# Kernel optimization log

Hardware: AMD Instinct MI355X
Metric: run time of the kernel (lower is better)

The kernel has to match this reference:

```python
import jax, jax.numpy as jnp
import numpy as np
import math

U_CONST = 0.5
FAC_DECAY = math.exp(-1.0 / 100.0)  # tau_fac = 100
DEP_DECAY = math.exp(-1.0 / 200.0)  # tau_dep = 200
BATCH, IN_F, OUT_F = 8192, 4096, 128


def setup_inputs() -> dict:
    key = jax.random.key(0)
    k1, k2 = jax.random.split(key)
    # binary spikes in {0,1} as float32
    pre_spike = jax.random.randint(k1, (BATCH, IN_F), 0, 2).astype(jnp.float32)
    # weight ~ U[0.25, 0.75) per torch.rand(out,in)*0.5 + 0.25
    weight = jax.random.uniform(k2, (OUT_F, IN_F), dtype=jnp.float32) * 0.5 + 0.25
    u = jnp.full((BATCH, IN_F), U_CONST, dtype=jnp.float32)  # facilitation state
    x = jnp.ones((BATCH, IN_F), dtype=jnp.float32)           # depression state
    return {"pre_spike": pre_spike, "weight": weight, "u": u, "x": x}


def reference(pre_spike, weight, u, x):
    # release probability per (batch, in_feature); fold onto pre_spike instead of
    # materializing the (batch, out, in) effective weight (same math).
    release_prob = u * x
    out = jnp.einsum('bi,oi->bo', pre_spike * release_prob, weight)  # [B, out]

    # STP state updates (facilitation then depression; x-update uses NEW u)
    u_fd = u * FAC_DECAY
    u_new = u_fd + U_CONST * (1.0 - u_fd) * pre_spike
    x_new = x * DEP_DECAY + (1.0 - x) * DEP_DECAY * (1.0 - pre_spike * u_new)
    return out, u_new, x_new
```

## Files before the change

kernel.cpp:

```cpp
#include <hip/hip_runtime.h>
#include <hip/hip_bf16.h>
#include <cstdint>

#define BATCH 8192
#define IN_F  4096
#define OUT_F 128
#define KSPLIT 16
#define KSLICE (IN_F / KSPLIT)
#define NKS    (KSLICE / 32)
#define FD 0.99004983374916811f
#define DD 0.99501247919268232f

typedef __attribute__((ext_vector_type(4))) float f32x4;
typedef __attribute__((ext_vector_type(8))) float f32x8;
typedef __attribute__((ext_vector_type(8))) short bf16x8;

__device__ __forceinline__ unsigned short f2bf(float f){
  union { float f; unsigned u; } v; v.f = f;
  unsigned u = v.u;
  return (unsigned short)((u + 0x7FFFu + ((u >> 16) & 1u)) >> 16);
}

__global__ __launch_bounds__(256) void prep_weight_kernel(const float* __restrict__ w,
                                                          unsigned short* __restrict__ wf){
  const int f  = blockIdx.x * 256 + threadIdx.x;
  const int l  = f & 63;
  const int ct = (f >> 6) & 7;
  const int ks = f >> 9;
  const int row = ct * 16 + (l & 15);
  const int k   = ks * 32 + ((l >> 4) << 3);
  const f32x4* src = reinterpret_cast<const f32x4*>(w + (size_t)row * IN_F + k);
  f32x4 a = src[0], b = src[1];
  union { bf16x8 v; unsigned short s[8]; } o;
  o.s[0]=f2bf(a[0]); o.s[1]=f2bf(a[1]); o.s[2]=f2bf(a[2]); o.s[3]=f2bf(a[3]);
  o.s[4]=f2bf(b[0]); o.s[5]=f2bf(b[1]); o.s[6]=f2bf(b[2]); o.s[7]=f2bf(b[3]);
  *reinterpret_cast<bf16x8*>(wf + (size_t)f * 8) = o.v;
}

template<bool WS>
__global__ __launch_bounds__(256, 4) void stp_fused_kernel(
    const float* __restrict__ pre, const float* __restrict__ uin,
    const float* __restrict__ xin, const float* __restrict__ w,
    const unsigned short* __restrict__ wf,
    float* __restrict__ out, float* __restrict__ un_out, float* __restrict__ xn_out)
{
  const int tid = threadIdx.x;
  const int wv  = tid >> 6;
  const int l   = tid & 63;

  const int kslice  = blockIdx.x & (KSPLIT - 1);
  const int rowBase = (blockIdx.x >> 4) * 64 + wv * 16;
  const int row     = rowBase + (l & 15);
  const size_t base = (size_t)row * IN_F + kslice * KSLICE + ((l >> 4) << 3);

  f32x4 acc[8];
  #pragma unroll
  for (int ct = 0; ct < 8; ++ct) acc[ct] = (f32x4){0.f,0.f,0.f,0.f};

  f32x8 sC = *reinterpret_cast<const f32x8*>(pre + base);
  f32x8 uC = *reinterpret_cast<const f32x8*>(uin + base);
  f32x8 xC = *reinterpret_cast<const f32x8*>(xin + base);

  for (int ks = 0; ks < NKS; ++ks){
    const size_t g   = base + (size_t)(ks << 5);
    const int    gks = kslice * NKS + ks;

    bf16x8 bf[8];
    if (WS){
      const bf16x8* wfp = reinterpret_cast<const bf16x8*>(wf);
      #pragma unroll
      for (int ct = 0; ct < 8; ++ct)
        bf[ct] = wfp[(size_t)((gks * 8 + ct) << 6) + l];
    } else {
      const int kg = gks * 32 + ((l >> 4) << 3);
      #pragma unroll
      for (int ct = 0; ct < 8; ++ct){
        const int r0 = ct * 16 + (l & 15);
        const f32x4* p = reinterpret_cast<const f32x4*>(w + (size_t)r0 * IN_F + kg);
        f32x4 a = p[0], b = p[1];
        union { bf16x8 v; unsigned short s[8]; } t;
        t.s[0]=f2bf(a[0]); t.s[1]=f2bf(a[1]); t.s[2]=f2bf(a[2]); t.s[3]=f2bf(a[3]);
        t.s[4]=f2bf(b[0]); t.s[5]=f2bf(b[1]); t.s[6]=f2bf(b[2]); t.s[7]=f2bf(b[3]);
        bf[ct] = t.v;
      }
    }

    f32x8 sN, uN, xN;
    if (ks + 1 < NKS){
      const size_t gn = base + (size_t)((ks + 1) << 5);
      sN = *reinterpret_cast<const f32x8*>(pre + gn);
      uN = *reinterpret_cast<const f32x8*>(uin + gn);
      xN = *reinterpret_cast<const f32x8*>(xin + gn);
    }

    f32x8 un, xn;
    union { bf16x8 v; unsigned short s[8]; } af;
    #pragma unroll
    for (int j = 0; j < 8; ++j){
      const float s = sC[j], u = uC[j], x = xC[j];
      af.s[j] = f2bf(u * x * s);
      const float ufd = u * FD;
      const float unj = ufd + 0.5f * (1.0f - ufd) * s;
      un[j] = unj;
      xn[j] = x * DD + (1.0f - x) * DD * (1.0f - s * unj);
    }
    *reinterpret_cast<f32x8*>(un_out + g) = un;
    *reinterpret_cast<f32x8*>(xn_out + g) = xn;

    #pragma unroll
    for (int ct = 0; ct < 8; ++ct)
      acc[ct] = __builtin_amdgcn_mfma_f32_16x16x32_bf16(af.v, bf[ct], acc[ct], 0, 0, 0);

    sC = sN; uC = uN; xC = xN;
  }

  const int col0 = l & 15;
  const int r0   = rowBase + ((l >> 4) << 2);
  #pragma unroll
  for (int ct = 0; ct < 8; ++ct){
    #pragma unroll
    for (int rg = 0; rg < 4; ++rg){
      unsafeAtomicAdd(&out[(size_t)(r0 + rg) * OUT_F + ct * 16 + col0], acc[ct][rg]);
    }
  }
}

extern "C" void kernel_launch(void* const* d_in, const int* in_sizes, int n_in,
                              void* d_out, int out_size, void* d_ws, size_t ws_size,
                              hipStream_t stream){
  const float* pre = (const float*)d_in[0];
  const float* w   = (const float*)d_in[1];
  const float* u   = (const float*)d_in[2];
  const float* x   = (const float*)d_in[3];
  float* out    = (float*)d_out;
  float* un_out = out + (size_t)BATCH * OUT_F;
  float* xn_out = un_out + (size_t)BATCH * IN_F;
  unsigned short* wf = (unsigned short*)d_ws;

  hipMemsetAsync(out, 0, (size_t)BATCH * OUT_F * sizeof(float), stream);

  const bool use_ws = (ws_size >= (size_t)(1 << 20));
  const int grid = (BATCH / 64) * KSPLIT;
  if (use_ws){
    prep_weight_kernel<<<256, 256, 0, stream>>>(w, wf);
    stp_fused_kernel<true><<<grid, 256, 0, stream>>>(pre, u, x, w, wf, out, un_out, xn_out);
  } else {
    stp_fused_kernel<false><<<grid, 256, 0, stream>>>(pre, u, x, w, nullptr, out, un_out, xn_out);
  }
}
```

Baseline: 187.7 us.

## Split K across waves in-block with LDS reduction, drop atomics and weight prep

After: 324.1 us. 1.73x slower.

```diff
diff --git a/kernel.cpp b/kernel.cpp
--- a/kernel.cpp
+++ b/kernel.cpp
@@ -5,9 +5,6 @@
 #define BATCH 8192
 #define IN_F  4096
 #define OUT_F 128
-#define KSPLIT 16
-#define KSLICE (IN_F / KSPLIT)
-#define NKS    (KSLICE / 32)
 #define FD 0.99004983374916811f
 #define DD 0.99501247919268232f
 
@@ -21,37 +18,18 @@
   return (unsigned short)((u + 0x7FFFu + ((u >> 16) & 1u)) >> 16);
 }
 
-__global__ __launch_bounds__(256) void prep_weight_kernel(const float* __restrict__ w,
-                                                          unsigned short* __restrict__ wf){
-  const int f  = blockIdx.x * 256 + threadIdx.x;
-  const int l  = f & 63;
-  const int ct = (f >> 6) & 7;
-  const int ks = f >> 9;
-  const int row = ct * 16 + (l & 15);
-  const int k   = ks * 32 + ((l >> 4) << 3);
-  const f32x4* src = reinterpret_cast<const f32x4*>(w + (size_t)row * IN_F + k);
-  f32x4 a = src[0], b = src[1];
-  union { bf16x8 v; unsigned short s[8]; } o;
-  o.s[0]=f2bf(a[0]); o.s[1]=f2bf(a[1]); o.s[2]=f2bf(a[2]); o.s[3]=f2bf(a[3]);
-  o.s[4]=f2bf(b[0]); o.s[5]=f2bf(b[1]); o.s[6]=f2bf(b[2]); o.s[7]=f2bf(b[3]);
-  *reinterpret_cast<bf16x8*>(wf + (size_t)f * 8) = o.v;
-}
-
-template<bool WS>
-__global__ __launch_bounds__(256, 4) void stp_fused_kernel(
+__global__ __launch_bounds__(512, 4) void stp_fused3(
     const float* __restrict__ pre, const float* __restrict__ uin,
     const float* __restrict__ xin, const float* __restrict__ w,
-    const unsigned short* __restrict__ wf,
     float* __restrict__ out, float* __restrict__ un_out, float* __restrict__ xn_out)
 {
+  __shared__ float red[8][16 * OUT_F];
+
   const int tid = threadIdx.x;
   const int wv  = tid >> 6;
   const int l   = tid & 63;
-
-  const int kslice  = blockIdx.x & (KSPLIT - 1);
-  const int rowBase = (blockIdx.x >> 4) * 64 + wv * 16;
-  const int row     = rowBase + (l & 15);
-  const size_t base = (size_t)row * IN_F + kslice * KSLICE + ((l >> 4) << 3);
+  const int rowBase = blockIdx.x * 16;
+  const size_t base = (size_t)(rowBase + (l & 15)) * IN_F + wv * 512 + ((l >> 4) << 3);
 
   f32x4 acc[8];
   #pragma unroll
@@ -61,33 +39,26 @@
   f32x8 uC = *reinterpret_cast<const f32x8*>(uin + base);
   f32x8 xC = *reinterpret_cast<const f32x8*>(xin + base);
 
-  for (int ks = 0; ks < NKS; ++ks){
+  for (int ks = 0; ks < 16; ++ks){
     const size_t g   = base + (size_t)(ks << 5);
-    const int    gks = kslice * NKS + ks;
+    const int    gks = (wv << 4) + ks;
+    const int    kg  = (gks << 5) + ((l >> 4) << 3);
 
     bf16x8 bf[8];
-    if (WS){
-      const bf16x8* wfp = reinterpret_cast<const bf16x8*>(wf);
-      #pragma unroll
-      for (int ct = 0; ct < 8; ++ct)
-        bf[ct] = wfp[(size_t)((gks * 8 + ct) << 6) + l];
-    } else {
-      const int kg = gks * 32 + ((l >> 4) << 3);
-      #pragma unroll
-      for (int ct = 0; ct < 8; ++ct){
-        const int r0 = ct * 16 + (l & 15);
-        const f32x4* p = reinterpret_cast<const f32x4*>(w + (size_t)r0 * IN_F + kg);
-        f32x4 a = p[0], b = p[1];
-        union { bf16x8 v; unsigned short s[8]; } t;
-        t.s[0]=f2bf(a[0]); t.s[1]=f2bf(a[1]); t.s[2]=f2bf(a[2]); t.s[3]=f2bf(a[3]);
-        t.s[4]=f2bf(b[0]); t.s[5]=f2bf(b[1]); t.s[6]=f2bf(b[2]); t.s[7]=f2bf(b[3]);
-        bf[ct] = t.v;
-      }
+    #pragma unroll
+    for (int ct = 0; ct < 8; ++ct){
+      const int r0 = ct * 16 + (l & 15);
+      const f32x4* p = reinterpret_cast<const f32x4*>(w + (size_t)r0 * IN_F + kg);
+      f32x4 a = p[0], b = p[1];
+      union { bf16x8 v; unsigned short s[8]; } t;
+      t.s[0]=f2bf(a[0]); t.s[1]=f2bf(a[1]); t.s[2]=f2bf(a[2]); t.s[3]=f2bf(a[3]);
+      t.s[4]=f2bf(b[0]); t.s[5]=f2bf(b[1]); t.s[6]=f2bf(b[2]); t.s[7]=f2bf(b[3]);
+      bf[ct] = t.v;
     }
 
     f32x8 sN, uN, xN;
-    if (ks + 1 < NKS){
-      const size_t gn = base + (size_t)((ks + 1) << 5);
+    if (ks < 15){
+      const size_t gn = g + 32;
       sN = *reinterpret_cast<const f32x8*>(pre + gn);
       uN = *reinterpret_cast<const f32x8*>(uin + gn);
       xN = *reinterpret_cast<const f32x8*>(xin + gn);
@@ -104,8 +75,8 @@
       un[j] = unj;
       xn[j] = x * DD + (1.0f - x) * DD * (1.0f - s * unj);
     }
-    *reinterpret_cast<f32x8*>(un_out + g) = un;
-    *reinterpret_cast<f32x8*>(xn_out + g) = xn;
+    __builtin_nontemporal_store(un, reinterpret_cast<f32x8*>(un_out + g));
+    __builtin_nontemporal_store(xn, reinterpret_cast<f32x8*>(xn_out + g));
 
     #pragma unroll
     for (int ct = 0; ct < 8; ++ct)
@@ -114,15 +85,21 @@
     sC = sN; uC = uN; xC = xN;
   }
 
-  const int col0 = l & 15;
-  const int r0   = rowBase + ((l >> 4) << 2);
   #pragma unroll
   for (int ct = 0; ct < 8; ++ct){
     #pragma unroll
     for (int rg = 0; rg < 4; ++rg){
-      unsafeAtomicAdd(&out[(size_t)(r0 + rg) * OUT_F + ct * 16 + col0], acc[ct][rg]);
+      red[wv][(((l >> 4) << 2) + rg) * OUT_F + ct * 16 + (l & 15)] = acc[ct][rg];
     }
   }
+  __syncthreads();
+
+  const int e = tid << 2;
+  f32x4 sum = *reinterpret_cast<const f32x4*>(&red[0][e]);
+  #pragma unroll
+  for (int wq = 1; wq < 8; ++wq)
+    sum += *reinterpret_cast<const f32x4*>(&red[wq][e]);
+  *reinterpret_cast<f32x4*>(out + (size_t)rowBase * OUT_F + e) = sum;
 }
 
 extern "C" void kernel_launch(void* const* d_in, const int* in_sizes, int n_in,
@@ -135,16 +112,6 @@
   float* out    = (float*)d_out;
   float* un_out = out + (size_t)BATCH * OUT_F;
   float* xn_out = un_out + (size_t)BATCH * IN_F;
-  unsigned short* wf = (unsigned short*)d_ws;
 
-  hipMemsetAsync(out, 0, (size_t)BATCH * OUT_F * sizeof(float), stream);
-
-  const bool use_ws = (ws_size >= (size_t)(1 << 20));
-  const int grid = (BATCH / 64) * KSPLIT;
-  if (use_ws){
-    prep_weight_kernel<<<256, 256, 0, stream>>>(w, wf);
-    stp_fused_kernel<true><<<grid, 256, 0, stream>>>(pre, u, x, w, wf, out, un_out, xn_out);
-  } else {
-    stp_fused_kernel<false><<<grid, 256, 0, stream>>>(pre, u, x, w, nullptr, out, un_out, xn_out);
-  }
+  stp_fused3<<<BATCH / 16, 512, 0, stream>>>(pre, u, x, w, out, un_out, xn_out);
 }
```

## Deepen prefetch to two stages, halve K-split, drop non-workspace fallback

Applied to the files above, without the earlier changes.

Result: faster. 179.7 us (-4.3%).

```diff
diff --git a/kernel.cpp b/kernel.cpp
--- a/kernel.cpp
+++ b/kernel.cpp
@@ -5,7 +5,7 @@
 #define BATCH 8192
 #define IN_F  4096
 #define OUT_F 128
-#define KSPLIT 16
+#define KSPLIT 8
 #define KSLICE (IN_F / KSPLIT)
 #define NKS    (KSLICE / 32)
 #define FD 0.99004983374916811f
@@ -37,11 +37,9 @@
   *reinterpret_cast<bf16x8*>(wf + (size_t)f * 8) = o.v;
 }
 
-template<bool WS>
-__global__ __launch_bounds__(256, 4) void stp_fused_kernel(
+__global__ __launch_bounds__(256, 3) void stp_fused7(
     const float* __restrict__ pre, const float* __restrict__ uin,
-    const float* __restrict__ xin, const float* __restrict__ w,
-    const unsigned short* __restrict__ wf,
+    const float* __restrict__ xin, const unsigned short* __restrict__ wf,
     float* __restrict__ out, float* __restrict__ un_out, float* __restrict__ xn_out)
 {
   const int tid = threadIdx.x;
@@ -49,69 +47,61 @@
   const int l   = tid & 63;
 
   const int kslice  = blockIdx.x & (KSPLIT - 1);
-  const int rowBase = (blockIdx.x >> 4) * 64 + wv * 16;
-  const int row     = rowBase + (l & 15);
-  const size_t base = (size_t)row * IN_F + kslice * KSLICE + ((l >> 4) << 3);
+  const int rowBase = (blockIdx.x >> 3) * 64 + wv * 16;
+  const size_t base = (size_t)(rowBase + (l & 15)) * IN_F + kslice * KSLICE + ((l >> 4) << 3);
+
+  const bf16x8* wfp = reinterpret_cast<const bf16x8*>(wf);
 
   f32x4 acc[8];
   #pragma unroll
   for (int ct = 0; ct < 8; ++ct) acc[ct] = (f32x4){0.f,0.f,0.f,0.f};
 
-  f32x8 sC = *reinterpret_cast<const f32x8*>(pre + base);
-  f32x8 uC = *reinterpret_cast<const f32x8*>(uin + base);
-  f32x8 xC = *reinterpret_cast<const f32x8*>(xin + base);
+  f32x8 s0 = *reinterpret_cast<const f32x8*>(pre + base);
+  f32x8 u0 = *reinterpret_cast<const f32x8*>(uin + base);
+  f32x8 x0 = *reinterpret_cast<const f32x8*>(xin + base);
+  f32x8 s1 = *reinterpret_cast<const f32x8*>(pre + base + 32);
+  f32x8 u1 = *reinterpret_cast<const f32x8*>(uin + base + 32);
+  f32x8 x1 = *reinterpret_cast<const f32x8*>(xin + base + 32);
 
+  #pragma unroll 2
   for (int ks = 0; ks < NKS; ++ks){
     const size_t g   = base + (size_t)(ks << 5);
     const int    gks = kslice * NKS + ks;
 
-    bf16x8 bf[8];
-    if (WS){
-      const bf16x8* wfp = reinterpret_cast<const bf16x8*>(wf);
-      #pragma unroll
-      for (int ct = 0; ct < 8; ++ct)
-        bf[ct] = wfp[(size_t)((gks * 8 + ct) << 6) + l];
-    } else {
-      const int kg = gks * 32 + ((l >> 4) << 3);
-      #pragma unroll
-      for (int ct = 0; ct < 8; ++ct){
-        const int r0 = ct * 16 + (l & 15);
-        const f32x4* p = reinterpret_cast<const f32x4*>(w + (size_t)r0 * IN_F + kg);
-        f32x4 a = p[0], b = p[1];
-        union { bf16x8 v; unsigned short s[8]; } t;
-        t.s[0]=f2bf(a[0]); t.s[1]=f2bf(a[1]); t.s[2]=f2bf(a[2]); t.s[3]=f2bf(a[3]);
-        t.s[4]=f2bf(b[0]); t.s[5]=f2bf(b[1]); t.s[6]=f2bf(b[2]); t.s[7]=f2bf(b[3]);
-        bf[ct] = t.v;
-      }
-    }
-
-    f32x8 sN, uN, xN;
-    if (ks + 1 < NKS){
-      const size_t gn = base + (size_t)((ks + 1) << 5);
-      sN = *reinterpret_cast<const f32x8*>(pre + gn);
-      uN = *reinterpret_cast<const f32x8*>(uin + gn);
-      xN = *reinterpret_cast<const f32x8*>(xin + gn);
-    }
+    bf16x8 b[8];
+    #pragma unroll
+    for (int ct = 0; ct < 8; ++ct)
+      b[ct] = wfp[(size_t)((gks * 8 + ct) << 6) + l];
 
     f32x8 un, xn;
     union { bf16x8 v; unsigned short s[8]; } af;
     #pragma unroll
     for (int j = 0; j < 8; ++j){
-      const float s = sC[j], u = uC[j], x = xC[j];
+      const float s = s0[j], u = u0[j], x = x0[j];
       af.s[j] = f2bf(u * x * s);
       const float ufd = u * FD;
       const float unj = ufd + 0.5f * (1.0f - ufd) * s;
       un[j] = unj;
       xn[j] = x * DD + (1.0f - x) * DD * (1.0f - s * unj);
     }
+
     *reinterpret_cast<f32x8*>(un_out + g) = un;
     *reinterpret_cast<f32x8*>(xn_out + g) = xn;
 
+    f32x8 s2, u2, x2;
+    if (ks + 2 < NKS){
+      const size_t g2 = base + (size_t)((ks + 2) << 5);
+      s2 = *reinterpret_cast<const f32x8*>(pre + g2);
+      u2 = *reinterpret_cast<const f32x8*>(uin + g2);
+      x2 = *reinterpret_cast<const f32x8*>(xin + g2);
+    }
+
     #pragma unroll
     for (int ct = 0; ct < 8; ++ct)
-      acc[ct] = __builtin_amdgcn_mfma_f32_16x16x32_bf16(af.v, bf[ct], acc[ct], 0, 0, 0);
+      acc[ct] = __builtin_amdgcn_mfma_f32_16x16x32_bf16(af.v, b[ct], acc[ct], 0, 0, 0);
 
-    sC = sN; uC = uN; xC = xN;
+    s0 = s1; u0 = u1; x0 = x1;
+    s1 = s2; u1 = u2; x1 = x2;
   }
 
   const int col0 = l & 15;
@@ -139,12 +129,6 @@
 
   hipMemsetAsync(out, 0, (size_t)BATCH * OUT_F * sizeof(float), stream);
 
-  const bool use_ws = (ws_size >= (size_t)(1 << 20));
-  const int grid = (BATCH / 64) * KSPLIT;
-  if (use_ws){
-    prep_weight_kernel<<<256, 256, 0, stream>>>(w, wf);
-    stp_fused_kernel<true><<<grid, 256, 0, stream>>>(pre, u, x, w, wf, out, un_out, xn_out);
-  } else {
-    stp_fused_kernel<false><<<grid, 256, 0, stream>>>(pre, u, x, w, nullptr, out, un_out, xn_out);
-  }
+  prep_weight_kernel<<<256, 256, 0, stream>>>(w, wf);
+  stp_fused7<<<(BATCH / 64) * KSPLIT, 256, 0, stream>>>(pre, u, x, wf, out, un_out, xn_out);
 }
```
